# Performance work log

Hardware: AMD Instinct MI355X
Metric: run time of the kernel (lower is better)

Reference implementation:

```python
import jax, jax.numpy as jnp
import numpy as np

B, G, P, C = 16, 14, 16, 3          # batch, patch grid (14x14), patch size, channels
D, DI, HM, L = 384, 768, 1536, 12   # embed_dim, d_inner=expand*D, mlp_hidden=4*D, depth


def _ln(x, g, b, eps=1e-5):
    m = x.mean(-1, keepdims=True)
    v = ((x - m) ** 2).mean(-1, keepdims=True)
    return (x - m) * jax.lax.rsqrt(v + eps) * g + b


def _lin_attn(seq, wi, bi, wo, bo, g, b):
    # LinearAttention fallback: gated pointwise MLP (SiLU(z)*sigmoid(gate)) + LN + proj_out
    zg = seq @ wi + bi
    z, gate = jnp.split(zg, 2, axis=-1)
    z = jax.nn.silu(z) * jax.nn.sigmoid(gate)
    return _ln(z, g, b) @ wo + bo


def setup_inputs():
    key = jax.random.key(0)
    ks = jax.random.split(key, 8)
    def w(k, shape, s=0.02):
        return (jax.random.normal(k, shape) * s).astype(jnp.float32)
    return {
        'x': jax.random.normal(ks[0], (B, C, G * P, G * P), jnp.float32),
        'patch_w': w(ks[1], (C * P * P, D)), 'patch_b': jnp.zeros((D,), jnp.float32),
        'pe_g': jnp.ones((D,), jnp.float32), 'pe_b': jnp.zeros((D,), jnp.float32),
        'pos': w(ks[2], (1, G * G, D)),
        'n1_g': jnp.ones((L, D), jnp.float32), 'n1_b': jnp.zeros((L, D), jnp.float32),
        'pi_w': w(ks[3], (L, 4, D, 2 * DI)), 'pi_b': jnp.zeros((L, 4, 2 * DI), jnp.float32),
        'po_w': w(ks[4], (L, 4, DI, D)), 'po_b': jnp.zeros((L, 4, D), jnp.float32),
        'la_g': jnp.ones((L, 4, DI), jnp.float32), 'la_b': jnp.zeros((L, 4, DI), jnp.float32),
        'mg_w': w(ks[5], (L, 4 * D, D)), 'mg_b': jnp.zeros((L, D), jnp.float32),
        'sn_g': jnp.ones((L, D), jnp.float32), 'sn_b': jnp.zeros((L, D), jnp.float32),
        'n2_g': jnp.ones((L, D), jnp.float32), 'n2_b': jnp.zeros((L, D), jnp.float32),
        'm1_w': w(ks[6], (L, D, HM)), 'm1_b': jnp.zeros((L, HM), jnp.float32),
        'm2_w': w(ks[7], (L, HM, D)), 'm2_b': jnp.zeros((L, D), jnp.float32),
        'fin_g': jnp.ones((D,), jnp.float32), 'fin_b': jnp.zeros((D,), jnp.float32),
    }


def reference(x, patch_w, patch_b, pe_g, pe_b, pos, n1_g, n1_b, pi_w, pi_b, po_w, po_b,
              la_g, la_b, mg_w, mg_b, sn_g, sn_b, n2_g, n2_b, m1_w, m1_b, m2_w, m2_b,
              fin_g, fin_b):
    Bsz = x.shape[0]
    # Patch embed: non-overlapping conv == per-patch linear projection
    patches = x.reshape(Bsz, C, G, P, G, P).transpose(0, 2, 4, 1, 3, 5).reshape(Bsz, G, G, C * P * P)
    h = _ln(patches @ patch_w + patch_b, pe_g, pe_b)          # [B, G, G, D]
    h = (h.reshape(Bsz, G * G, D) + pos).reshape(Bsz, G, G, D)  # pos embed (no interp: grid==base)
    for l in range(L):
        hn = _ln(h, n1_g[l], n1_b[l])
        # 4-direction scan sequences (-> <- down up)
        ht = hn.transpose(0, 2, 1, 3)
        seqs = [hn.reshape(Bsz, G * G, D),
                hn[:, ::-1, ::-1].reshape(Bsz, G * G, D),
                ht.reshape(Bsz, G * G, D),
                ht[:, ::-1, ::-1].reshape(Bsz, G * G, D)]
        outs = []
        for i in range(4):
            o = _lin_attn(seqs[i], pi_w[l, i], pi_b[l, i], po_w[l, i], po_b[l, i], la_g[l, i], la_b[l, i])
            if i == 1:
                o = o[:, ::-1]
            elif i == 2:
                o = o.reshape(Bsz, G, G, D).transpose(0, 2, 1, 3).reshape(Bsz, G * G, D)
            elif i == 3:
                o = o[:, ::-1].reshape(Bsz, G, G, D).transpose(0, 2, 1, 3).reshape(Bsz, G * G, D)
            outs.append(o)
        merged = jnp.concatenate(outs, axis=-1) @ mg_w[l] + mg_b[l]
        merged = _ln(merged, sn_g[l], sn_b[l]).reshape(Bsz, G, G, D)
        h = h + merged
        hn2 = _ln(h, n2_g[l], n2_b[l])
        h = h + (jax.nn.gelu(hn2 @ m1_w[l] + m1_b[l], approximate=False) @ m2_w[l] + m2_b[l])
    return _ln(h.reshape(Bsz, G * G, D), fin_g, fin_b)  # dense features [B, N, D]
```

## Files before the change

kernel.cpp:

```cpp
#include <hip/hip_runtime.h>
#include <math.h>

typedef unsigned short u16;
typedef __bf16 bf16x8 __attribute__((ext_vector_type(8)));
typedef float f32x4 __attribute__((ext_vector_type(4)));

#define L_   12
#define NTOK 3136
#define MP   3200

__device__ __forceinline__ float b2f(u16 v){ return __builtin_bit_cast(float, (unsigned)v<<16); }
__device__ __forceinline__ u16 f2b(float f){
    unsigned u = __builtin_bit_cast(unsigned, f);
    u += 0x7fffu + ((u>>16)&1u);
    return (u16)(u>>16);
}
__device__ __forceinline__ float wsum(float v){
    #pragma unroll
    for (int o=32;o;o>>=1) v += __shfl_xor(v,o);
    return v;
}
__device__ __forceinline__ void gl_lds16(const void* g, void* l){
    __builtin_amdgcn_global_load_lds(
        (const __attribute__((address_space(1))) void*)g,
        (__attribute__((address_space(3))) void*)l, 16, 0, 0);
}

__device__ __host__ __forceinline__ int rho16(int c){
    return (c < 768) ? (((c>>4)<<5) + (c&15)) : ((((c-768)>>4)<<5) + 16 + ((c-768)&15));
}

__global__ __launch_bounds__(256) void k_transpose(const float* __restrict__ src,
                                                   u16* __restrict__ dst, int R, int C){
    __shared__ float t[32][33];
    long long base = (long long)blockIdx.z * R * C;
    int c0 = blockIdx.x<<5, r0 = blockIdx.y<<5;
    int tx = threadIdx.x & 31, ty = threadIdx.x >> 5;
    #pragma unroll
    for (int i=0;i<32;i+=8)
        t[ty+i][tx] = src[base + (long long)(r0+ty+i)*C + c0 + tx];
    __syncthreads();
    #pragma unroll
    for (int i=0;i<32;i+=8)
        dst[base + (long long)(c0+ty+i)*R + r0 + tx] = f2b(t[tx][ty+i]);
}

__global__ __launch_bounds__(256) void k_transpose_pi(const float* __restrict__ src,
                                                      u16* __restrict__ dst){
    const int R = 384, C = 1536;
    __shared__ float t[32][33];
    long long base = (long long)blockIdx.z * R * C;
    int c0 = blockIdx.x<<5, r0 = blockIdx.y<<5;
    int tx = threadIdx.x & 31, ty = threadIdx.x >> 5;
    #pragma unroll
    for (int i=0;i<32;i+=8)
        t[ty+i][tx] = src[base + (long long)(r0+ty+i)*C + c0 + tx];
    __syncthreads();
    #pragma unroll
    for (int i=0;i<32;i+=8){
        int c = c0 + ty + i;
        dst[base + (long long)rho16(c)*R + r0 + tx] = f2b(t[tx][ty+i]);
    }
}

__global__ __launch_bounds__(256) void k_bi(const float* __restrict__ pi_b, float* __restrict__ out){
    int idx = blockIdx.x*256 + threadIdx.x;
    if (idx >= 48*1536) return;
    int slab = idx / 1536, c = idx - slab*1536;
    int l = slab >> 2, dir = slab & 3;
    out[(long long)l*6144 + dir*1536 + rho16(c)] = pi_b[idx];
}

__global__ __launch_bounds__(384) void k_cvt_bw(const float* __restrict__ po_w,
                                                const float* __restrict__ la_g,
                                                const float* __restrict__ la_b,
                                                u16* __restrict__ po_bf,
                                                float* __restrict__ tvec){
    int z = blockIdx.x, chunk = blockIdx.y;
    int i = threadIdx.x;
    const float* pw = po_w + (long long)z*294912;
    u16* ob = po_bf + (long long)z*294912;
    const float* lb = la_b + (long long)z*768;
    const float* lg = la_g + (long long)z*768;
    float s = 0.f;
    int c0 = chunk*128;
    for (int ci=c0; ci<c0+128; ci++){
        float v = pw[(long long)ci*384 + i];
        s = fmaf(lb[ci], v, s);
        ob[(long long)ci*384 + i] = f2b(v * lg[ci]);
    }
    atomicAdd(tvec + (long long)z*384 + i, s);
}

__global__ __launch_bounds__(384) void k_bw2(const float* __restrict__ tvec,
                                             const float* __restrict__ po_b,
                                             const float* __restrict__ mg_w,
                                             float* __restrict__ fullb){
    int z = blockIdx.x, chunk = blockIdx.y;
    int l = z>>2, dir = z&3;
    int i = threadIdx.x;
    const float* mw = mg_w + (long long)l*589824 + (long long)dir*147456;
    const float* tv = tvec + (long long)z*384;
    const float* pb = po_b + (long long)z*384;
    float s = 0.f;
    int m0 = chunk*64;
    for (int m=m0; m<m0+64; m++) s = fmaf(tv[m]+pb[m], mw[(long long)m*384 + i], s);
    atomicAdd(fullb + (long long)l*384 + i, s);
}

__global__ __launch_bounds__(256) void k_stats(const u16* __restrict__ gated,
                                               float* __restrict__ st){
    int unit = blockIdx.x*4 + (threadIdx.x>>6);
    int lane = threadIdx.x & 63;
    const u16* p = gated + (long long)(unit>>2)*3072 + (unit&3)*768;
    float s1 = 0.f, s2 = 0.f;
    #pragma unroll
    for (int i=0;i<3;i++){
        ushort4 v = *reinterpret_cast<const ushort4*>(p + i*256 + lane*4);
        const u16* a = (const u16*)&v;
        #pragma unroll
        for (int q=0;q<4;q++){ float f = b2f(a[q]); s1 += f; s2 += f*f; }
    }
    s1 = wsum(s1); s2 = wsum(s2);
    if (lane==0){
        st[(long long)unit*2]   = s1;
        st[(long long)unit*2+1] = s2;
    }
}

__global__ __launch_bounds__(256) void k_patches(const float* __restrict__ x, u16* __restrict__ out){
    int idx = blockIdx.x*256 + threadIdx.x;
    int row = idx / 768, col = idx - row*768;
    float v = 0.f;
    if (row < NTOK){
        int b = row / 196, t = row - b*196;
        int gi = t / 14, gj = t - gi*14;
        int c = col >> 8, rem = col & 255, pi = rem >> 4, pj = rem & 15;
        v = x[((long long)(b*3 + c)*224 + gi*16 + pi)*224 + gj*16 + pj];
    }
    out[idx] = f2b(v);
}

template<int EPI, int BM, int BN>
__global__ __launch_bounds__(256) void gemm_tn(
    const u16* __restrict__ A, int lda, long long aSh, long long aSl,
    const u16* __restrict__ Bt, int ldb, long long bSh, long long bSl,
    const float* __restrict__ bias, long long biasSh, int splitBias,
    void* __restrict__ Cbase, int ldc, long long cSh, long long cSl,
    int K, int zshift, const float* __restrict__ aux, float* __restrict__ auxw)
{
    constexpr int AI = BM/32;
    constexpr int BI = BN/32;
    constexpr int NF = (BM==128) ? BN/32 : BN/64;
    constexpr int LP = AI + BI;
    int z = blockIdx.z;
    int zh = z >> zshift, zl = z - (zh << zshift);
    const u16* Az  = A  + zh*aSh + zl*aSl;
    const u16* Btz = Bt + zh*bSh + zl*bSl;
    bool addb = bias && (!splitBias || zl == 0);
    long long cOff = zh*cSh + zl*cSl;
    int m0 = blockIdx.y*BM, n0 = blockIdx.x*BN;

    __shared__ u16 As[2][BM*64];
    __shared__ u16 Bs[2][BN*64];

    int tid = threadIdx.x;
    int lane = tid & 63;
    int w = tid >> 6;
    int wrb = (BM==128) ? (w>>1)*64 : 0;
    int wcb = (BM==128) ? (w&1)*(BN/2) : w*(BN/4);
    int rsub = lane >> 3, csub = lane & 7;
    int scol = ((csub ^ rsub) << 3);
    int kxor = (lane & 7) << 4;

    const u16* ga[AI]; const u16* gb[BI]; int loa[AI], lob[BI];
    #pragma unroll
    for (int j=0;j<AI;j++){
        int r = j*32 + w*8 + rsub;
        ga[j] = Az + (long long)(m0 + r)*lda + scol;
        loa[j] = (j*32 + w*8)*64;
    }
    #pragma unroll
    for (int j=0;j<BI;j++){
        int r = j*32 + w*8 + rsub;
        gb[j] = Btz + (long long)(n0 + r)*ldb + scol;
        lob[j] = (j*32 + w*8)*64;
    }

    f32x4 acc[4][NF];
    #pragma unroll
    for (int m=0;m<4;m++)
        #pragma unroll
        for (int n=0;n<NF;n++) acc[m][n] = (f32x4){0.f,0.f,0.f,0.f};

    int nkt = K >> 6;

    auto stage = [&](int ko, int p){
        #pragma unroll
        for (int j=0;j<AI;j++) gl_lds16(ga[j] + ko, &As[p][loa[j]]);
        #pragma unroll
        for (int j=0;j<BI;j++) gl_lds16(gb[j] + ko, &Bs[p][lob[j]]);
    };

    stage(0, 0);
    stage(64, 1);

    auto step = [&](int kt, int p){
        if (kt == nkt-1)            asm volatile("s_waitcnt vmcnt(0)" ::: "memory");
        else if constexpr (LP==6)   asm volatile("s_waitcnt vmcnt(6)" ::: "memory");
        else if constexpr (LP==8)   asm volatile("s_waitcnt vmcnt(8)" ::: "memory");
        else                        asm volatile("s_waitcnt vmcnt(10)" ::: "memory");
        __builtin_amdgcn_s_barrier();
        const char* as = (const char*)As[p];
        const char* bs = (const char*)Bs[p];
        bf16x8 af[2][4], bfr[2][NF];
        #pragma unroll
        for (int kk=0; kk<2; ++kk){
            int kb = ((kk*32 + ((lane>>4)<<3))*2) ^ kxor;
            #pragma unroll
            for (int m=0;m<4;m++){
                int r = wrb + m*16 + (lane&15);
                af[kk][m] = *reinterpret_cast<const bf16x8*>(as + r*128 + kb);
            }
            #pragma unroll
            for (int n=0;n<NF;n++){
                int r = wcb + n*16 + (lane&15);
                bfr[kk][n] = *reinterpret_cast<const bf16x8*>(bs + r*128 + kb);
            }
        }
        asm volatile("s_waitcnt lgkmcnt(0)" ::: "memory");
        __builtin_amdgcn_sched_barrier(0);
        __builtin_amdgcn_s_barrier();
        if (kt+2 < nkt) stage((kt+2)<<6, p);
        #pragma unroll
        for (int kk=0; kk<2; ++kk)
            #pragma unroll
            for (int m=0;m<4;m++)
                #pragma unroll
                for (int n=0;n<NF;n++)
                    acc[m][n] = __builtin_amdgcn_mfma_f32_16x16x32_bf16(af[kk][m], bfr[kk][n], acc[m][n], 0,0,0);
    };

    for (int kt=0; kt<nkt; kt+=2){ step(kt, 0); step(kt+1, 1); }

    int rbase = m0 + wrb;
    int nbase = n0 + wcb;
    if (EPI==3){
        int dir = n0/1536;
        #pragma unroll
        for (int np2=0; np2<NF/2; ++np2){
            int ncz = nbase + (np2*2)*16 + (lane&15);
            int pz  = ncz - dir*1536;
            int ci  = ((pz>>5)<<4) + (pz&15);
            float bz = addb ? bias[ncz]      : 0.f;
            float bg = addb ? bias[ncz+16]   : 0.f;
            #pragma unroll
            for (int m=0;m<4;m++){
                #pragma unroll
                for (int r4=0;r4<4;r4++){
                    int row = rbase + m*16 + ((lane>>4)<<2) + r4;
                    float vz = acc[m][np2*2][r4]   + bz;
                    float vg = acc[m][np2*2+1][r4] + bg;
                    float gv = vz / ((1.f+__expf(-vz))*(1.f+__expf(-vg)));
                    ((u16*)Cbase)[(long long)row*3072 + dir*768 + ci] = f2b(gv);
                }
            }
        }
    } else if (EPI==4){
        #pragma unroll
        for (int m=0;m<4;m++){
            #pragma unroll
            for (int r4=0;r4<4;r4++){
                int row = rbase + m*16 + ((lane>>4)<<2) + r4;
                float st1 = aux[((long long)row*4 + zl)*2];
                float st2 = aux[((long long)row*4 + zl)*2 + 1];
                float mu = st1*(1.f/768.f);
                float rs = rsqrtf(st2*(1.f/768.f) - mu*mu + 1e-5f);
                #pragma unroll
                for (int n=0;n<NF;n++){
                    int ncol = nbase + n*16 + (lane&15);
                    float gsv = bias[(long long)zl*384 + ncol];
                    ((float*)Cbase)[(long long)row*ldc + ncol + cOff] = (acc[m][n][r4] - mu*gsv)*rs;
                }
            }
        }
    } else if (EPI==5){
        #pragma unroll
        for (int m=0;m<4;m++){
            #pragma unroll
            for (int r4=0;r4<4;r4++){
                int row = rbase + m*16 + ((lane>>4)<<2) + r4;
                float s = 0.f;
                #pragma unroll
                for (int n=0;n<NF;n++){
                    int ncol = nbase + n*16 + (lane&15);
                    u16 rv = f2b(acc[m][n][r4]);
                    ((u16*)Cbase)[(long long)row*ldc + ncol + cOff] = rv;
                    s += b2f(rv);
                }
                #pragma unroll
                for (int o=1;o<16;o<<=1) s += __shfl_xor(s, o);
                if ((lane&15)==0) atomicAdd(auxw + (long long)z*384 + row, s);
            }
        }
    } else {
        #pragma unroll
        for (int m=0;m<4;m++){
            #pragma unroll
            for (int n=0;n<NF;n++){
                int ncol = nbase + n*16 + (lane&15);
                float bv = addb ? bias[zh*biasSh + ncol] : 0.f;
                #pragma unroll
                for (int r4=0;r4<4;r4++){
                    int row = rbase + m*16 + ((lane>>4)<<2) + r4;
                    float v = acc[m][n][r4] + bv;
                    long long idx = (long long)row*ldc + ncol + cOff;
                    if (EPI==0)      ((u16*)Cbase)[idx] = f2b(v);
                    else if (EPI==1){
                        float gl = 0.5f*v*(1.f + erff(v*0.70710678118f));
                        ((u16*)Cbase)[idx] = f2b(gl);
                    }
                    else             ((float*)Cbase)[idx] = v;
                }
            }
        }
    }
}

template<int MODE>
__global__ __launch_bounds__(256) void k_addln(float* __restrict__ h,
        const float* __restrict__ parts, int np,
        const float* __restrict__ g, const float* __restrict__ b, void* __restrict__ out){
    int row = blockIdx.x*4 + (threadIdx.x>>6);
    int lane = threadIdx.x & 63;
    float* hp = h + (long long)row*384;
    float v[6]; float s = 0.f;
    #pragma unroll
    for (int i=0;i<6;i++){
        int c = lane + i*64;
        float t = hp[c];
        for (int p=0;p<np;p++) t += parts[(long long)p*MP*384 + (long long)row*384 + c];
        v[i] = t; s += t;
    }
    if (MODE==0 && np){
        #pragma unroll
        for (int i=0;i<6;i++) hp[lane + i*64] = v[i];
    }
    float mu = wsum(s)*(1.f/384.f);
    float q = 0.f;
    #pragma unroll
    for (int i=0;i<6;i++){ float d = v[i]-mu; q += d*d; }
    float rs = rsqrtf(wsum(q)*(1.f/384.f) + 1e-5f);
    if (MODE==0){
        u16* op = (u16*)out + (long long)row*384;
        #pragma unroll
        for (int i=0;i<6;i++){ int c = lane + i*64; op[c] = f2b((v[i]-mu)*rs*g[c] + b[c]); }
    } else {
        float* op = (float*)out + (long long)row*384;
        #pragma unroll
        for (int i=0;i<6;i++){ int c = lane + i*64; op[c] = (v[i]-mu)*rs*g[c] + b[c]; }
    }
}

__global__ __launch_bounds__(256) void k_pe_ln(const float* __restrict__ parts,
        const float* __restrict__ g, const float* __restrict__ b,
        const float* __restrict__ pos, float* __restrict__ h,
        const float* __restrict__ n1g, const float* __restrict__ n1b,
        u16* __restrict__ hn){
    int row = blockIdx.x*4 + (threadIdx.x>>6);
    int lane = threadIdx.x & 63;
    float v[6]; float s = 0.f;
    #pragma unroll
    for (int i=0;i<6;i++){
        int c = lane + i*64;
        float t = parts[(long long)row*384 + c] + parts[(long long)MP*384 + (long long)row*384 + c];
        v[i] = t; s += t;
    }
    float mu = wsum(s)*(1.f/384.f);
    float q = 0.f;
    #pragma unroll
    for (int i=0;i<6;i++){ float d = v[i]-mu; q += d*d; }
    float rs = rsqrtf(wsum(q)*(1.f/384.f) + 1e-5f);
    int t = row % 196;
    const float* pp = pos + (long long)t*384;
    float* op = h + (long long)row*384;
    float hv[6]; float s2 = 0.f;
    #pragma unroll
    for (int i=0;i<6;i++){
        int c = lane + i*64;
        float nv = (v[i]-mu)*rs*g[c] + b[c] + pp[c];
        op[c] = nv; hv[i] = nv; s2 += nv;
    }
    float mu2 = wsum(s2)*(1.f/384.f);
    float q2 = 0.f;
    #pragma unroll
    for (int i=0;i<6;i++){ float d = hv[i]-mu2; q2 += d*d; }
    float rs2 = rsqrtf(wsum(q2)*(1.f/384.f) + 1e-5f);
    u16* hp = hn + (long long)row*384;
    #pragma unroll
    for (int i=0;i<6;i++){ int c = lane + i*64; hp[c] = f2b((hv[i]-mu2)*rs2*n1g[c] + n1b[c]); }
}

__global__ __launch_bounds__(256) void k_sn_ln(const float* __restrict__ parts,
        const float* __restrict__ fullb, const float* __restrict__ mgb,
        const float* __restrict__ sg, const float* __restrict__ sb,
        float* __restrict__ h,
        const float* __restrict__ n2g, const float* __restrict__ n2b,
        u16* __restrict__ hn2){
    int row = blockIdx.x*4 + (threadIdx.x>>6);
    int lane = threadIdx.x & 63;
    float v[6]; float s = 0.f;
    #pragma unroll
    for (int i=0;i<6;i++){
        int c = lane + i*64;
        long long o = (long long)row*384 + c;
        float t = mgb[c] + fullb[c];
        #pragma unroll
        for (int p=0;p<4;p++) t += parts[(long long)p*MP*384 + o];
        v[i] = t; s += t;
    }
    float mu = wsum(s)*(1.f/384.f);
    float q = 0.f;
    #pragma unroll
    for (int i=0;i<6;i++){ float d = v[i]-mu; q += d*d; }
    float rs = rsqrtf(wsum(q)*(1.f/384.f) + 1e-5f);
    float* hp = h + (long long)row*384;
    float hv[6]; float s2 = 0.f;
    #pragma unroll
    for (int i=0;i<6;i++){
        int c = lane + i*64;
        float nv = hp[c] + (v[i]-mu)*rs*sg[c] + sb[c];
        hp[c] = nv; hv[i] = nv; s2 += nv;
    }
    float mu2 = wsum(s2)*(1.f/384.f);
    float q2 = 0.f;
    #pragma unroll
    for (int i=0;i<6;i++){ float d = hv[i]-mu2; q2 += d*d; }
    float rs2 = rsqrtf(wsum(q2)*(1.f/384.f) + 1e-5f);
    u16* op = hn2 + (long long)row*384;
    #pragma unroll
    for (int i=0;i<6;i++){ int c = lane + i*64; op[c] = f2b((hv[i]-mu2)*rs2*n2g[c] + n2b[c]); }
}

extern "C" void kernel_launch(void* const* d_in, const int* in_sizes, int n_in,
                              void* d_out, int out_size, void* d_ws, size_t ws_size,
                              hipStream_t stream)
{
    const float* x      = (const float*)d_in[0];
    const float* patch_w= (const float*)d_in[1];
    const float* patch_b= (const float*)d_in[2];
    const float* pe_g   = (const float*)d_in[3];
    const float* pe_b   = (const float*)d_in[4];
    const float* pos    = (const float*)d_in[5];
    const float* n1_g   = (const float*)d_in[6];
    const float* n1_b   = (const float*)d_in[7];
    const float* pi_w   = (const float*)d_in[8];
    const float* pi_b   = (const float*)d_in[9];
    const float* po_w   = (const float*)d_in[10];
    const float* po_b   = (const float*)d_in[11];
    const float* la_g   = (const float*)d_in[12];
    const float* la_b   = (const float*)d_in[13];
    const float* mg_w   = (const float*)d_in[14];
    const float* mg_b   = (const float*)d_in[15];
    const float* sn_g   = (const float*)d_in[16];
    const float* sn_b   = (const float*)d_in[17];
    const float* n2_g   = (const float*)d_in[18];
    const float* n2_b   = (const float*)d_in[19];
    const float* m1_w   = (const float*)d_in[20];
    const float* m1_b   = (const float*)d_in[21];
    const float* m2_w   = (const float*)d_in[22];
    const float* m2_b   = (const float*)d_in[23];
    const float* fin_g  = (const float*)d_in[24];
    const float* fin_b  = (const float*)d_in[25];

    char* wptr = (char*)d_ws;
    auto carve = [&](long long elems, int esz)->void*{
        void* p = (void*)wptr;
        wptr += ((elems*(long long)esz + 255)/256)*256;
        return p;
    };

    u16* wt_pi  = (u16*)carve(28311552, 2);
    u16* wt_mgr = (u16*)carve(7077888, 2);
    u16* wt_m1  = (u16*)carve(7077888, 2);
    u16* wt_m2  = (u16*)carve(7077888, 2);
    u16* wt_pe  = (u16*)carve(294912, 2);
    u16* po_bf  = (u16*)carve(14155776, 2);
    u16* WcT    = (u16*)carve(14155776, 2);
    float* Gs   = (float*)carve(48*384, 4);
    float* tvec = (float*)carve(48*384, 4);
    float* fullb= (float*)carve(12*384, 4);
    size_t zbytes = (size_t)((char*)(fullb + 12*384) - (char*)Gs);
    float* stats= (float*)carve(MP*8, 4);
    float* pib_i= (float*)carve(12*6144, 4);
    float* h    = (float*)carve((long long)MP*384, 4);
    float* parts= (float*)carve(4LL*MP*384, 4);
    u16* patches= (u16*)carve((long long)MP*768, 2);
    u16* hn     = (u16*)carve((long long)MP*384, 2);
    u16* gated  = (u16*)carve((long long)MP*3072, 2);
    u16* outs   = (u16*)carve((long long)MP*1536, 2);

    dim3 blk(256);

    hipMemsetAsync(Gs, 0, zbytes, stream);
    k_transpose_pi<<<dim3(48,12,48), blk, 0, stream>>>(pi_w, wt_pi);
    k_bi<<<dim3((48*1536+255)/256), blk, 0, stream>>>(pi_b, pib_i);
    k_transpose<<<dim3(12,12,48), blk, 0, stream>>>(mg_w,   wt_mgr, 384, 384);
    k_transpose<<<dim3(48,12,12), blk, 0, stream>>>(m1_w,   wt_m1, 384, 1536);
    k_transpose<<<dim3(12,48,12), blk, 0, stream>>>(m2_w,   wt_m2, 1536, 384);
    k_transpose<<<dim3(12,24,1),  blk, 0, stream>>>(patch_w,wt_pe, 768, 384);
    k_cvt_bw<<<dim3(48,6), dim3(384), 0, stream>>>(po_w, la_g, la_b, po_bf, tvec);
    k_bw2<<<dim3(48,6), dim3(384), 0, stream>>>(tvec, po_b, mg_w, fullb);
    gemm_tn<5,128,128><<<dim3(6,3,48), blk, 0, stream>>>(
        wt_mgr, 384, 589824LL, 147456LL,
        po_bf,  384, 1179648LL, 294912LL,
        nullptr, 0, 0,
        WcT, 3072, 1179648LL, 768LL, 384, 2, nullptr, Gs);

    k_patches<<<dim3(MP*768/256), blk, 0, stream>>>(x, patches);
    gemm_tn<2,64,128><<<dim3(3,50,2), blk, 0, stream>>>(
        patches, 768, 0, 384,
        wt_pe,   768, 0, 384,
        patch_b, 0, 1,
        parts, 384, 0, (long long)MP*384, 384, 1, nullptr, nullptr);
    k_pe_ln<<<dim3(MP/4), blk, 0, stream>>>(parts, pe_g, pe_b, pos, h, n1_g, n1_b, hn);

    for (int l=0; l<L_; ++l){
        gemm_tn<3,128,128><<<dim3(48,25,1), blk, 0, stream>>>(
            hn, 384, 0, 0,
            wt_pi + (long long)l*2359296, 384, 0, 0,
            pib_i + (long long)l*6144, 0, 0,
            gated, 3072, 0, 0, 384, 0, nullptr, nullptr);
        k_stats<<<dim3(MP), blk, 0, stream>>>(gated, stats);
        gemm_tn<4,64,128><<<dim3(3,50,4), blk, 0, stream>>>(
            gated, 3072, 0, 768,
            WcT + (long long)l*1179648, 3072, 0, 768,
            Gs + (long long)l*1536, 0, 0,
            parts, 384, 0, (long long)MP*384, 768, 2, stats, nullptr);
        k_sn_ln<<<dim3(MP/4), blk, 0, stream>>>(parts,
                                                fullb + (long long)l*384, mg_b + l*384,
                                                sn_g + l*384, sn_b + l*384,
                                                h, n2_g + l*384, n2_b + l*384, hn);
        gemm_tn<1,64,128><<<dim3(12,50,1), blk, 0, stream>>>(
            hn, 384, 0, 0,
            wt_m1 + (long long)l*589824, 384, 0, 0,
            m1_b + (long long)l*1536, 0, 0,
            outs, 1536, 0, 0, 384, 0, nullptr, nullptr);
        gemm_tn<2,64,128><<<dim3(3,50,2), blk, 0, stream>>>(
            outs, 1536, 0, 768,
            wt_m2 + (long long)l*589824, 1536, 0, 768,
            m2_b + l*384, 0, 1,
            parts, 384, 0, (long long)MP*384, 768, 1, nullptr, nullptr);
        if (l < L_-1)
            k_addln<0><<<dim3(MP/4), blk, 0, stream>>>(h, parts, 2,
                n1_g + (l+1)*384, n1_b + (l+1)*384, hn);
        else
            k_addln<1><<<dim3(NTOK/4), blk, 0, stream>>>(h, parts, 2,
                fin_g, fin_b, (float*)d_out);
    }
}
```

Baseline: 1.307 ms.

## Replace split-K partial buffers with atomic accumulation into output

The merge GEMM (four directions) now atomically adds into a single accumulator that k_stats zeroes, instead of writing four partial slices that k_sn_ln sums. The MLP down-projection GEMM gets a new epilogue that atomically adds its two K-split halves plus bias straight into the residual h, so k_addln no longer reads the parts buffers. This removes the writes and re-reads of the partial buffers. In exchange it adds float atomic contention, makes summation order nondeterministic, and relies on k_stats covering every row of the accumulator when zeroing it.

New measurement: 1.408 ms. +7.7%, slower.

```diff
diff --git a/kernel.cpp b/kernel.cpp
--- a/kernel.cpp
+++ b/kernel.cpp
@@ -109,8 +109,12 @@
 }
 
 __global__ __launch_bounds__(256) void k_stats(const u16* __restrict__ gated,
-                                               float* __restrict__ st){
-    int unit = blockIdx.x*4 + (threadIdx.x>>6);
+                                               float* __restrict__ st,
+                                               float* __restrict__ macc){
+    int b = blockIdx.x;
+    for (int i = threadIdx.x; i < 384; i += 256)
+        macc[(long long)b*384 + i] = 0.f;
+    int unit = b*4 + (threadIdx.x>>6);
     int lane = threadIdx.x & 63;
     const u16* p = gated + (long long)(unit>>2)*3072 + (unit&3)*768;
     float s1 = 0.f, s2 = 0.f;
@@ -280,7 +284,7 @@
                 for (int n=0;n<NF;n++){
                     int ncol = nbase + n*16 + (lane&15);
                     float gsv = bias[(long long)zl*384 + ncol];
-                    ((float*)Cbase)[(long long)row*ldc + ncol + cOff] = (acc[m][n][r4] - mu*gsv)*rs;
+                    atomicAdd(&((float*)Cbase)[(long long)row*ldc + ncol], (acc[m][n][r4] - mu*gsv)*rs);
                 }
             }
         }
@@ -301,6 +305,20 @@
                 #pragma unroll
                 for (int o=1;o<16;o<<=1) s += __shfl_xor(s, o);
                 if ((lane&15)==0) atomicAdd(auxw + (long long)z*384 + row, s);
+            }
+        }
+    } else if (EPI==6){
+        #pragma unroll
+        for (int m=0;m<4;m++){
+            #pragma unroll
+            for (int n=0;n<NF;n++){
+                int ncol = nbase + n*16 + (lane&15);
+                float bv = addb ? bias[ncol] : 0.f;
+                #pragma unroll
+                for (int r4=0;r4<4;r4++){
+                    int row = rbase + m*16 + ((lane>>4)<<2) + r4;
+                    atomicAdd(&((float*)Cbase)[(long long)row*ldc + ncol], acc[m][n][r4] + bv);
+                }
             }
         }
     } else {
@@ -401,7 +419,7 @@
     for (int i=0;i<6;i++){ int c = lane + i*64; hp[c] = f2b((hv[i]-mu2)*rs2*n1g[c] + n1b[c]); }
 }
 
-__global__ __launch_bounds__(256) void k_sn_ln(const float* __restrict__ parts,
+__global__ __launch_bounds__(256) void k_sn_ln(const float* __restrict__ macc,
         const float* __restrict__ fullb, const float* __restrict__ mgb,
         const float* __restrict__ sg, const float* __restrict__ sb,
         float* __restrict__ h,
@@ -413,10 +431,7 @@
     #pragma unroll
     for (int i=0;i<6;i++){
         int c = lane + i*64;
-        long long o = (long long)row*384 + c;
-        float t = mgb[c] + fullb[c];
-        #pragma unroll
-        for (int p=0;p<4;p++) t += parts[(long long)p*MP*384 + o];
+        float t = mgb[c] + fullb[c] + macc[(long long)row*384 + c];
         v[i] = t; s += t;
     }
     float mu = wsum(s)*(1.f/384.f);
@@ -494,7 +509,8 @@
     float* stats= (float*)carve(MP*8, 4);
     float* pib_i= (float*)carve(12*6144, 4);
     float* h    = (float*)carve((long long)MP*384, 4);
-    float* parts= (float*)carve(4LL*MP*384, 4);
+    float* macc = (float*)carve((long long)MP*384, 4);
+    float* parts= (float*)carve(2LL*MP*384, 4);
     u16* patches= (u16*)carve((long long)MP*768, 2);
     u16* hn     = (u16*)carve((long long)MP*384, 2);
     u16* gated  = (u16*)carve((long long)MP*3072, 2);
@@ -531,13 +547,13 @@
             wt_pi + (long long)l*2359296, 384, 0, 0,
             pib_i + (long long)l*6144, 0, 0,
             gated, 3072, 0, 0, 384, 0, nullptr, nullptr);
-        k_stats<<<dim3(MP), blk, 0, stream>>>(gated, stats);
+        k_stats<<<dim3(MP), blk, 0, stream>>>(gated, stats, macc);
         gemm_tn<4,64,128><<<dim3(3,50,4), blk, 0, stream>>>(
             gated, 3072, 0, 768,
             WcT + (long long)l*1179648, 3072, 0, 768,
             Gs + (long long)l*1536, 0, 0,
-            parts, 384, 0, (long long)MP*384, 768, 2, stats, nullptr);
-        k_sn_ln<<<dim3(MP/4), blk, 0, stream>>>(parts,
+            macc, 384, 0, 0, 768, 2, stats, nullptr);
+        k_sn_ln<<<dim3(MP/4), blk, 0, stream>>>(macc,
                                                 fullb + (long long)l*384, mg_b + l*384,
                                                 sn_g + l*384, sn_b + l*384,
                                                 h, n2_g + l*384, n2_b + l*384, hn);
@@ -546,16 +562,16 @@
             wt_m1 + (long long)l*589824, 384, 0, 0,
             m1_b + (long long)l*1536, 0, 0,
             outs, 1536, 0, 0, 384, 0, nullptr, nullptr);
-        gemm_tn<2,64,128><<<dim3(3,50,2), blk, 0, stream>>>(
+        gemm_tn<6,64,128><<<dim3(3,50,2), blk, 0, stream>>>(
             outs, 1536, 0, 768,
             wt_m2 + (long long)l*589824, 1536, 0, 768,
             m2_b + l*384, 0, 1,
-            parts, 384, 0, (long long)MP*384, 768, 1, nullptr, nullptr);
+            h, 384, 0, 0, 768, 1, nullptr, nullptr);
         if (l < L_-1)
-            k_addln<0><<<dim3(MP/4), blk, 0, stream>>>(h, parts, 2,
+            k_addln<0><<<dim3(MP/4), blk, 0, stream>>>(h, nullptr, 0,
                 n1_g + (l+1)*384, n1_b + (l+1)*384, hn);
         else
-            k_addln<1><<<dim3(NTOK/4), blk, 0, stream>>>(h, parts, 2,
+            k_addln<1><<<dim3(NTOK/4), blk, 0, stream>>>(h, nullptr, 0,
                 fin_g, fin_b, (float*)d_out);
     }
 }
```

## Replace double-buffered LDS staging with single buffer in GEMM

Applied to the files above, without the earlier changes.

Switches the GEMM main loop from a two-deep LDS ring (prefetch two k-tiles ahead) to a single LDS buffer that loads only the next tile, issued after fragments are copied into registers. This halves shared memory per block, which could allow more resident blocks per CU. The cost is a shallower prefetch, with each iteration waiting for all outstanding global loads (vmcnt(0)), so global-load latency is less hidden behind MFMA work.

Result: faster. 1.258 ms (-3.7%).

```diff
diff --git a/kernel.cpp b/kernel.cpp
--- a/kernel.cpp
+++ b/kernel.cpp
@@ -152,7 +152,6 @@
     constexpr int AI = BM/32;
     constexpr int BI = BN/32;
     constexpr int NF = (BM==128) ? BN/32 : BN/64;
-    constexpr int LP = AI + BI;
     int z = blockIdx.z;
     int zh = z >> zshift, zl = z - (zh << zshift);
     const u16* Az  = A  + zh*aSh + zl*aSl;
@@ -161,8 +160,8 @@
     long long cOff = zh*cSh + zl*cSl;
     int m0 = blockIdx.y*BM, n0 = blockIdx.x*BN;
 
-    __shared__ u16 As[2][BM*64];
-    __shared__ u16 Bs[2][BN*64];
+    __shared__ u16 As[BM*64];
+    __shared__ u16 Bs[BN*64];
 
     int tid = threadIdx.x;
     int lane = tid & 63;
@@ -195,24 +194,20 @@
 
     int nkt = K >> 6;
 
-    auto stage = [&](int ko, int p){
-        #pragma unroll
-        for (int j=0;j<AI;j++) gl_lds16(ga[j] + ko, &As[p][loa[j]]);
-        #pragma unroll
-        for (int j=0;j<BI;j++) gl_lds16(gb[j] + ko, &Bs[p][lob[j]]);
+    auto stage = [&](int ko){
+        #pragma unroll
+        for (int j=0;j<AI;j++) gl_lds16(ga[j] + ko, &As[loa[j]]);
+        #pragma unroll
+        for (int j=0;j<BI;j++) gl_lds16(gb[j] + ko, &Bs[lob[j]]);
     };
 
-    stage(0, 0);
-    stage(64, 1);
-
-    auto step = [&](int kt, int p){
-        if (kt == nkt-1)            asm volatile("s_waitcnt vmcnt(0)" ::: "memory");
-        else if constexpr (LP==6)   asm volatile("s_waitcnt vmcnt(6)" ::: "memory");
-        else if constexpr (LP==8)   asm volatile("s_waitcnt vmcnt(8)" ::: "memory");
-        else                        asm volatile("s_waitcnt vmcnt(10)" ::: "memory");
+    stage(0);
+
+    for (int kt=0; kt<nkt; ++kt){
+        asm volatile("s_waitcnt vmcnt(0)" ::: "memory");
         __builtin_amdgcn_s_barrier();
-        const char* as = (const char*)As[p];
-        const char* bs = (const char*)Bs[p];
+        const char* as = (const char*)As;
+        const char* bs = (const char*)Bs;
         bf16x8 af[2][4], bfr[2][NF];
         #pragma unroll
         for (int kk=0; kk<2; ++kk){
@@ -231,7 +226,7 @@
         asm volatile("s_waitcnt lgkmcnt(0)" ::: "memory");
         __builtin_amdgcn_sched_barrier(0);
         __builtin_amdgcn_s_barrier();
-        if (kt+2 < nkt) stage((kt+2)<<6, p);
+        if (kt+1 < nkt) stage((kt+1)<<6);
         #pragma unroll
         for (int kk=0; kk<2; ++kk)
             #pragma unroll
@@ -239,9 +234,7 @@
                 #pragma unroll
                 for (int n=0;n<NF;n++)
                     acc[m][n] = __builtin_amdgcn_mfma_f32_16x16x32_bf16(af[kk][m], bfr[kk][n], acc[m][n], 0,0,0);
-    };
-
-    for (int kt=0; kt<nkt; kt+=2){ step(kt, 0); step(kt+1, 1); }
+    }
 
     int rbase = m0 + wrb;
     int nbase = n0 + wcb;
```
